# Kernel tuning notes

Measured on AMD Instinct MI355X. Metric: run time of the kernel, lower is better.

Reference implementation:

```python
import jax, jax.numpy as jnp
import numpy as np

ALPHA = 3.0   # config.model.hgnn_alpha
K = 16        # config.model.k_neighbors
S, N, E, D = 3, 8192, 1024, 512


def setup_inputs() -> dict:
    key = jax.random.key(0)
    k1, k2, k3 = jax.random.split(key, 3)
    x = jax.random.normal(k1, (1,), dtype=jnp.float32)  # only used for device in torch
    node_embed = jax.random.normal(k2, (S, N, D), dtype=jnp.float32)  # embednod tables
    edge_embed = jax.random.normal(k3, (S, E, D), dtype=jnp.float32)  # embedhy tables
    return {"x": x, "node_embed": node_embed, "edge_embed": edge_embed}


def reference(x, node_embed, edge_embed):
    # sim[s] = n_embed @ h_embed.T  -> [S, N, E]
    sim = jnp.einsum('snd,sed->sne', node_embed, edge_embed)
    # adj = softmax(relu(alpha * sim), dim=1 over hyperedges)
    adj = jax.nn.softmax(jax.nn.relu(ALPHA * sim), axis=-1)
    # top-k mask along hyperedge axis (scatter 1s at top-k indices per row)
    _, topk_idx = jax.lax.top_k(adj, K)  # [S, N, K]
    s_idx = jnp.arange(S)[:, None, None]
    n_idx = jnp.arange(N)[None, :, None]
    mask = jnp.zeros_like(adj).at[s_idx, n_idx, topk_idx].set(1.0)
    adj = adj * mask
    # hard threshold: binary incidence matrix per scale.
    # Original then drops all-zero hyperedge columns and returns nonzero
    # (node_idx, hyperedge_idx) pairs -- data-dependent shapes, so the dense
    # binary incidence [S, N, E] is the jit-compatible equivalent output;
    # the index lists are exactly its nonzero coordinates.
    hard = jnp.where(adj > 0.5, 1.0, 0.0)
    return hard
```

## Files before the change

kernel.cpp:

```cpp
#include <hip/hip_runtime.h>
#include <cmath>

#define SS 3
#define NN 8192
#define EE 1024
#define DD 512
#define ALPHA 3.0f
#define TAU 0.03f

typedef __attribute__((ext_vector_type(8))) short bf16x8;
typedef __attribute__((ext_vector_type(4))) float f32x4;

#define AS1(p) ((const __attribute__((address_space(1))) void*)(p))
#define AS3(p) ((__attribute__((address_space(3))) void*)(p))

__device__ __forceinline__ unsigned short f2bf(float x) {
    unsigned u = __float_as_uint(x);
    return (unsigned short)((u + 0x7fffu + ((u >> 16) & 1u)) >> 16);
}
__device__ __forceinline__ float bf2f(unsigned short h) {
    return __uint_as_float(((unsigned)h) << 16);
}

__device__ __forceinline__ void gload_lds16(const unsigned short* g, unsigned short* l) {
    __builtin_amdgcn_global_load_lds(AS1(g), AS3(l), 16, 0, 0);
}

__global__ __launch_bounds__(256)
void split_both_kernel(const float* __restrict__ node, const float* __restrict__ edge,
                       unsigned short* __restrict__ Ah, unsigned short* __restrict__ Al,
                       unsigned short* __restrict__ Bh, unsigned short* __restrict__ Bl)
{
    const int nA = SS * NN * DD / 4;
    const int nB = SS * EE * DD / 4;
    int i = blockIdx.x * blockDim.x + threadIdx.x;

    const float4* src;
    unsigned short* hi;
    unsigned short* lo;
    int idx;
    if (i < nA) {
        src = (const float4*)node; hi = Ah; lo = Al; idx = i;
    } else if (i < nA + nB) {
        src = (const float4*)edge; hi = Bh; lo = Bl; idx = i - nA;
    } else {
        return;
    }
    float4 v = src[idx];
    ushort4 h, l;
    h.x = f2bf(v.x); l.x = f2bf(v.x - bf2f(h.x));
    h.y = f2bf(v.y); l.y = f2bf(v.y - bf2f(h.y));
    h.z = f2bf(v.z); l.z = f2bf(v.z - bf2f(h.z));
    h.w = f2bf(v.w); l.w = f2bf(v.w - bf2f(h.w));
    ((ushort4*)hi)[idx] = h;
    ((ushort4*)lo)[idx] = l;
}

__global__ __launch_bounds__(256)
void gemm_mfma_kernel(const unsigned short* __restrict__ Ah,
                      const unsigned short* __restrict__ Al,
                      const unsigned short* __restrict__ Bh,
                      const unsigned short* __restrict__ Bl,
                      float* __restrict__ out)
{
    const int s  = blockIdx.z;
    const int m0 = blockIdx.x * 128;
    const int n0 = blockIdx.y * 128;

    const unsigned short* pAh = Ah + (size_t)s * NN * DD;
    const unsigned short* pAl = Al + (size_t)s * NN * DD;
    const unsigned short* pBh = Bh + (size_t)s * EE * DD;
    const unsigned short* pBl = Bl + (size_t)s * EE * DD;
    float* C = out + (size_t)s * NN * EE;

    __shared__ unsigned short lds[2 * 1024 * 8];

    const int t    = threadIdx.x;
    const int lane = t & 63;
    const int wid  = t >> 6;
    const int wm   = wid >> 1;
    const int wn   = wid & 1;
    const int fr   = lane & 15;
    const int kg   = lane >> 4;

    f32x4 acc[4][4];
#pragma unroll
    for (int i = 0; i < 4; ++i)
#pragma unroll
        for (int j = 0; j < 4; ++j) acc[i][j] = (f32x4){0.f, 0.f, 0.f, 0.f};

    for (int k0 = 0; k0 < DD; k0 += 32) {
#pragma unroll
        for (int i = 0; i < 8; ++i) {
            const int c    = i * 256 + t;
            const int pc   = c & 1023;
            const int row  = pc >> 3;
            const int slot = pc & 7;
            const int j    = slot ^ (row & 7);
            const unsigned short* src;
            if (c < 1024) {
                src = (j < 4) ? pAh + (size_t)(m0 + row) * DD + k0 + j * 8
                              : pAl + (size_t)(m0 + row) * DD + k0 + (j - 4) * 8;
            } else {
                src = (j < 4) ? pBh + (size_t)(n0 + row) * DD + k0 + j * 8
                              : pBl + (size_t)(n0 + row) * DD + k0 + (j - 4) * 8;
            }
            gload_lds16(src, &lds[c * 8]);
        }
        __syncthreads();

        bf16x8 ah[4], al[4], bh[4], bl[4];
#pragma unroll
        for (int i = 0; i < 4; ++i) {
            const int r = wm * 64 + i * 16 + fr;
            ah[i] = *(const bf16x8*)&lds[r * 64 + ((kg)     ^ (r & 7)) * 8];
            al[i] = *(const bf16x8*)&lds[r * 64 + ((4 + kg) ^ (r & 7)) * 8];
        }
#pragma unroll
        for (int j = 0; j < 4; ++j) {
            const int r = wn * 64 + j * 16 + fr;
            bh[j] = *(const bf16x8*)&lds[8192 + r * 64 + ((kg)     ^ (r & 7)) * 8];
            bl[j] = *(const bf16x8*)&lds[8192 + r * 64 + ((4 + kg) ^ (r & 7)) * 8];
        }
#pragma unroll
        for (int i = 0; i < 4; ++i)
#pragma unroll
            for (int j = 0; j < 4; ++j) {
                acc[i][j] = __builtin_amdgcn_mfma_f32_16x16x32_bf16(ah[i], bh[j], acc[i][j], 0, 0, 0);
                acc[i][j] = __builtin_amdgcn_mfma_f32_16x16x32_bf16(ah[i], bl[j], acc[i][j], 0, 0, 0);
                acc[i][j] = __builtin_amdgcn_mfma_f32_16x16x32_bf16(al[i], bh[j], acc[i][j], 0, 0, 0);
            }
        __syncthreads();
    }

#pragma unroll
    for (int i = 0; i < 4; ++i)
#pragma unroll
        for (int j = 0; j < 4; ++j) {
            const int col = n0 + wn * 64 + j * 16 + fr;
#pragma unroll
            for (int r = 0; r < 4; ++r) {
                const int row = m0 + wm * 64 + i * 16 + kg * 4 + r;
                C[(size_t)row * EE + col] = fmaxf(ALPHA * acc[i][j][r], 0.f);
            }
        }
}

__global__ void zero_count_kernel(int* __restrict__ count) {
    if (threadIdx.x == 0 && blockIdx.x == 0) count[0] = 0;
}

__global__ __launch_bounds__(256)
void softmax_threshold_flag_kernel(float* __restrict__ out,
                                   int* __restrict__ count,
                                   int* __restrict__ worklist)
{
    const int wave = threadIdx.x >> 6;
    const int lane = threadIdx.x & 63;
    const size_t row = (size_t)blockIdx.x * 4 + wave;
    float* p = out + row * EE;

    float z[16];
    float m = 0.f;
#pragma unroll
    for (int j = 0; j < 4; ++j) {
        float4 v = *(const float4*)(p + j * 256 + lane * 4);
        z[j*4+0] = v.x; z[j*4+1] = v.y; z[j*4+2] = v.z; z[j*4+3] = v.w;
        m = fmaxf(m, fmaxf(fmaxf(v.x, v.y), fmaxf(v.z, v.w)));
    }
#pragma unroll
    for (int off = 32; off >= 1; off >>= 1)
        m = fmaxf(m, __shfl_xor(m, off, 64));

    float e[16];
    float sum = 0.f;
#pragma unroll
    for (int j = 0; j < 16; ++j) {
        e[j] = expf(z[j] - m);
        sum += e[j];
    }
#pragma unroll
    for (int off = 32; off >= 1; off >>= 1)
        sum += __shfl_xor(sum, off, 64);

    const float thr = 0.5f * sum;
    const float T   = m + logf(thr);
    int lf = 0;
#pragma unroll
    for (int j = 0; j < 16; ++j)
        lf |= (fabsf(z[j] - T) < TAU) ? 1 : 0;

#pragma unroll
    for (int j = 0; j < 4; ++j) {
        float4 o;
        o.x = (e[j*4+0] > thr) ? 1.f : 0.f;
        o.y = (e[j*4+1] > thr) ? 1.f : 0.f;
        o.z = (e[j*4+2] > thr) ? 1.f : 0.f;
        o.w = (e[j*4+3] > thr) ? 1.f : 0.f;
        *(float4*)(p + j * 256 + lane * 4) = o;
    }
    const int anyf = __any(lf);
    if (anyf && lane == 0) {
        int idx = atomicAdd(count, 1);
        worklist[idx] = (int)row;
    }
}

__global__ __launch_bounds__(256)
void fixup_z_kernel(const float* __restrict__ node, const float* __restrict__ edge,
                    const int* __restrict__ count, const int* __restrict__ worklist,
                    float* __restrict__ zbuf, int zcap)
{
    __shared__ float sa[DD];
    const int t    = threadIdx.x;
    const int lane = t & 63;
    const int wid  = t >> 6;

    int nwork = count[0];
    if (nwork > zcap) nwork = zcap;
    const int items = nwork * 4;

    for (int item = blockIdx.x; item < items; item += gridDim.x) {
        const int w   = item >> 2;
        const int row = worklist[w];
        const int c0  = (item & 3) * 256;
        const int s   = row / NN;
        const float* a = node + (size_t)row * DD;
        const float* B = edge + (size_t)s * EE * DD;

        __syncthreads();
        if (t < DD / 4) ((float4*)sa)[t] = ((const float4*)a)[t];
        __syncthreads();

        const float4 va0 = ((const float4*)sa)[lane];
        const float4 va1 = ((const float4*)sa)[64 + lane];

        const int cbase = c0 + wid * 64;
        for (int g = 0; g < 16; ++g) {
            float acc[4];
#pragma unroll
            for (int j = 0; j < 4; ++j) {
                const float* b = B + (size_t)(cbase + g * 4 + j) * DD;
                float4 b0 = *(const float4*)(b + lane * 4);
                float4 b1 = *(const float4*)(b + 256 + lane * 4);
                float av;
                av = va0.x * b0.x;
                av = fmaf(va0.y, b0.y, av);
                av = fmaf(va0.z, b0.z, av);
                av = fmaf(va0.w, b0.w, av);
                av = fmaf(va1.x, b1.x, av);
                av = fmaf(va1.y, b1.y, av);
                av = fmaf(va1.z, b1.z, av);
                av = fmaf(va1.w, b1.w, av);
                acc[j] = av;
            }
#pragma unroll
            for (int off = 32; off >= 1; off >>= 1) {
#pragma unroll
                for (int j = 0; j < 4; ++j)
                    acc[j] += __shfl_xor(acc[j], off, 64);
            }
            if (lane == 0) {
#pragma unroll
                for (int j = 0; j < 4; ++j)
                    zbuf[(size_t)w * EE + cbase + g * 4 + j] = fmaxf(ALPHA * acc[j], 0.f);
            }
        }
    }
}

__global__ __launch_bounds__(256)
void fixup_finish_kernel(const float* __restrict__ zbuf,
                         const int* __restrict__ count, const int* __restrict__ worklist,
                         float* __restrict__ out, int zcap)
{
    const int lane = threadIdx.x & 63;
    const int wid  = threadIdx.x >> 6;
    int nwork = count[0];
    if (nwork > zcap) nwork = zcap;

    for (int w = blockIdx.x * 4 + wid; w < nwork; w += gridDim.x * 4) {
        const int row = worklist[w];
        const float* p = zbuf + (size_t)w * EE;

        float z[16];
        float m = 0.f;
#pragma unroll
        for (int j = 0; j < 4; ++j) {
            float4 v = *(const float4*)(p + j * 256 + lane * 4);
            z[j*4+0] = v.x; z[j*4+1] = v.y; z[j*4+2] = v.z; z[j*4+3] = v.w;
            m = fmaxf(m, fmaxf(fmaxf(v.x, v.y), fmaxf(v.z, v.w)));
        }
#pragma unroll
        for (int off = 32; off >= 1; off >>= 1)
            m = fmaxf(m, __shfl_xor(m, off, 64));

        float e[16], sum = 0.f;
#pragma unroll
        for (int j = 0; j < 16; ++j) { e[j] = expf(z[j] - m); sum += e[j]; }
#pragma unroll
        for (int off = 32; off >= 1; off >>= 1)
            sum += __shfl_xor(sum, off, 64);

        const float thr = 0.5f * sum;
        float* q = out + (size_t)row * EE;
#pragma unroll
        for (int j = 0; j < 4; ++j) {
            float4 o;
            o.x = (e[j*4+0] > thr) ? 1.f : 0.f;
            o.y = (e[j*4+1] > thr) ? 1.f : 0.f;
            o.z = (e[j*4+2] > thr) ? 1.f : 0.f;
            o.w = (e[j*4+3] > thr) ? 1.f : 0.f;
            *(float4*)(q + j * 256 + lane * 4) = o;
        }
    }
}

__global__ __launch_bounds__(256)
void fixup2_kernel(const float* __restrict__ node, const float* __restrict__ edge,
                   const int* __restrict__ count, const int* __restrict__ worklist,
                   float* __restrict__ out, int start)
{
    __shared__ float sa[DD];
    __shared__ float zrow[EE];
    __shared__ float red[8];

    const int t    = threadIdx.x;
    const int lane = t & 63;
    const int wid  = t >> 6;
    const int nwork = count[0];

    for (int w = start + blockIdx.x; w < nwork; w += gridDim.x) {
        const int row = worklist[w];
        const int s = row / NN;
        const float* a = node + (size_t)row * DD;
        const float* B = edge + (size_t)s * EE * DD;

        __syncthreads();
        if (t < DD / 4) ((float4*)sa)[t] = ((const float4*)a)[t];
        __syncthreads();

        float4 va0 = ((const float4*)sa)[lane];
        float4 va1 = ((const float4*)sa)[64 + lane];

        for (int c = wid; c < EE; c += 4) {
            const float* b = B + (size_t)c * DD;
            float4 b0 = *(const float4*)(b + lane * 4);
            float4 b1 = *(const float4*)(b + 256 + lane * 4);
            float acc;
            acc = va0.x * b0.x;
            acc = fmaf(va0.y, b0.y, acc);
            acc = fmaf(va0.z, b0.z, acc);
            acc = fmaf(va0.w, b0.w, acc);
            acc = fmaf(va1.x, b1.x, acc);
            acc = fmaf(va1.y, b1.y, acc);
            acc = fmaf(va1.z, b1.z, acc);
            acc = fmaf(va1.w, b1.w, acc);
#pragma unroll
            for (int off = 32; off >= 1; off >>= 1)
                acc += __shfl_xor(acc, off, 64);
            if (lane == 0) zrow[c] = fmaxf(ALPHA * acc, 0.f);
        }
        __syncthreads();

        float z[4], m = 0.f;
#pragma unroll
        for (int j = 0; j < 4; ++j) {
            z[j] = zrow[j * 256 + t];
            m = fmaxf(m, z[j]);
        }
#pragma unroll
        for (int off = 32; off >= 1; off >>= 1)
            m = fmaxf(m, __shfl_xor(m, off, 64));
        if (lane == 0) red[wid] = m;
        __syncthreads();
        m = fmaxf(fmaxf(red[0], red[1]), fmaxf(red[2], red[3]));

        float e[4], sum = 0.f;
#pragma unroll
        for (int j = 0; j < 4; ++j) { e[j] = expf(z[j] - m); sum += e[j]; }
#pragma unroll
        for (int off = 32; off >= 1; off >>= 1)
            sum += __shfl_xor(sum, off, 64);
        if (lane == 0) red[4 + wid] = sum;
        __syncthreads();
        sum = red[4] + red[5] + red[6] + red[7];

        const float thr = 0.5f * sum;
#pragma unroll
        for (int j = 0; j < 4; ++j)
            out[(size_t)row * EE + j * 256 + t] = (e[j] > thr) ? 1.f : 0.f;
        __syncthreads();
    }
}

#define BM 128
#define BN 128
#define BK 16
#define TM 8
#define TN 8

__global__ __launch_bounds__(256, 2)
void gemm_relu_kernel(const float* __restrict__ node,
                      const float* __restrict__ edge,
                      float* __restrict__ out)
{
    const int s  = blockIdx.z;
    const int m0 = blockIdx.y * BM;
    const int n0 = blockIdx.x * BN;

    const float* A = node + (size_t)s * NN * DD;
    const float* B = edge + (size_t)s * EE * DD;
    float*       C = out  + (size_t)s * NN * EE;

    __shared__ float As[BK][BM + 4];
    __shared__ float Bs[BK][BN + 4];

    const int tid = threadIdx.x;
    const int tx  = tid % 16;
    const int ty  = tid / 16;
    const int lrow = tid / 4;
    const int lcol = (tid % 4) * 4;

    float acc[TM][TN];
#pragma unroll
    for (int i = 0; i < TM; ++i)
#pragma unroll
        for (int j = 0; j < TN; ++j) acc[i][j] = 0.f;

    for (int k0 = 0; k0 < DD; k0 += BK) {
#pragma unroll
        for (int p = 0; p < 2; ++p) {
            const int r = lrow + p * 64;
            float4 v = *(const float4*)(A + (size_t)(m0 + r) * DD + k0 + lcol);
            As[lcol + 0][r] = v.x; As[lcol + 1][r] = v.y;
            As[lcol + 2][r] = v.z; As[lcol + 3][r] = v.w;
            float4 w = *(const float4*)(B + (size_t)(n0 + r) * DD + k0 + lcol);
            Bs[lcol + 0][r] = w.x; Bs[lcol + 1][r] = w.y;
            Bs[lcol + 2][r] = w.z; Bs[lcol + 3][r] = w.w;
        }
        __syncthreads();
#pragma unroll
        for (int k = 0; k < BK; ++k) {
            float a[TM], b[TN];
            float4 a0 = *(const float4*)&As[k][ty * 8];
            float4 a1 = *(const float4*)&As[k][ty * 8 + 4];
            a[0]=a0.x; a[1]=a0.y; a[2]=a0.z; a[3]=a0.w;
            a[4]=a1.x; a[5]=a1.y; a[6]=a1.z; a[7]=a1.w;
            float4 b0 = *(const float4*)&Bs[k][tx * 8];
            float4 b1 = *(const float4*)&Bs[k][tx * 8 + 4];
            b[0]=b0.x; b[1]=b0.y; b[2]=b0.z; b[3]=b0.w;
            b[4]=b1.x; b[5]=b1.y; b[6]=b1.z; b[7]=b1.w;
#pragma unroll
            for (int i = 0; i < TM; ++i)
#pragma unroll
                for (int j = 0; j < TN; ++j)
                    acc[i][j] = fmaf(a[i], b[j], acc[i][j]);
        }
        __syncthreads();
    }
#pragma unroll
    for (int i = 0; i < TM; ++i) {
        const size_t row = (size_t)(m0 + ty * 8 + i);
        float4 o0, o1;
        o0.x = fmaxf(ALPHA * acc[i][0], 0.f);
        o0.y = fmaxf(ALPHA * acc[i][1], 0.f);
        o0.z = fmaxf(ALPHA * acc[i][2], 0.f);
        o0.w = fmaxf(ALPHA * acc[i][3], 0.f);
        o1.x = fmaxf(ALPHA * acc[i][4], 0.f);
        o1.y = fmaxf(ALPHA * acc[i][5], 0.f);
        o1.z = fmaxf(ALPHA * acc[i][6], 0.f);
        o1.w = fmaxf(ALPHA * acc[i][7], 0.f);
        *(float4*)(C + row * EE + n0 + tx * 8)     = o0;
        *(float4*)(C + row * EE + n0 + tx * 8 + 4) = o1;
    }
}

__global__ __launch_bounds__(256)
void softmax_threshold_kernel(float* __restrict__ out)
{
    const int wave = threadIdx.x >> 6;
    const int lane = threadIdx.x & 63;
    const size_t row = (size_t)blockIdx.x * 4 + wave;
    float* p = out + row * EE;

    float z[16];
    float m = 0.f;
#pragma unroll
    for (int j = 0; j < 4; ++j) {
        float4 v = *(const float4*)(p + j * 256 + lane * 4);
        z[j*4+0] = v.x; z[j*4+1] = v.y; z[j*4+2] = v.z; z[j*4+3] = v.w;
        m = fmaxf(m, fmaxf(fmaxf(v.x, v.y), fmaxf(v.z, v.w)));
    }
#pragma unroll
    for (int off = 32; off >= 1; off >>= 1)
        m = fmaxf(m, __shfl_xor(m, off, 64));
    float e[16], sum = 0.f;
#pragma unroll
    for (int j = 0; j < 16; ++j) { e[j] = expf(z[j] - m); sum += e[j]; }
#pragma unroll
    for (int off = 32; off >= 1; off >>= 1)
        sum += __shfl_xor(sum, off, 64);
    const float thr = 0.5f * sum;
#pragma unroll
    for (int j = 0; j < 4; ++j) {
        float4 o;
        o.x = (e[j*4+0] > thr) ? 1.f : 0.f;
        o.y = (e[j*4+1] > thr) ? 1.f : 0.f;
        o.z = (e[j*4+2] > thr) ? 1.f : 0.f;
        o.w = (e[j*4+3] > thr) ? 1.f : 0.f;
        *(float4*)(p + j * 256 + lane * 4) = o;
    }
}

extern "C" void kernel_launch(void* const* d_in, const int* in_sizes, int n_in,
                              void* d_out, int out_size, void* d_ws, size_t ws_size,
                              hipStream_t stream) {
    const float* node = (const float*)d_in[1];
    const float* edge = (const float*)d_in[2];
    float* out = (float*)d_out;

    const size_t SAe = (size_t)SS * NN * DD;
    const size_t SBe = (size_t)SS * EE * DD;
    const size_t split_bytes = (2 * SAe + 2 * SBe) * 2;
    const size_t wl_bytes    = (size_t)(SS * NN + 1) * 4;
    const size_t base_need   = split_bytes + wl_bytes;

    if (ws_size >= base_need) {
        unsigned short* Ah = (unsigned short*)d_ws;
        unsigned short* Al = Ah + SAe;
        unsigned short* Bh = Al + SAe;
        unsigned short* Bl = Bh + SBe;
        int* count    = (int*)(Bl + SBe);
        int* worklist = count + 1;

        const size_t zoff = (base_need + 255) & ~(size_t)255;
        int zcap = 0;
        if (ws_size > zoff) {
            size_t zc = (ws_size - zoff) / ((size_t)EE * 4);
            zcap = (int)(zc > 4096 ? 4096 : zc);
        }
        float* zbuf = (float*)((char*)d_ws + zoff);

        const int n4 = (int)((SAe + SBe) / 4);
        split_both_kernel<<<(n4 + 255) / 256, 256, 0, stream>>>(node, edge, Ah, Al, Bh, Bl);

        zero_count_kernel<<<1, 64, 0, stream>>>(count);

        dim3 g1(NN / 128, EE / 128, SS);
        gemm_mfma_kernel<<<g1, 256, 0, stream>>>(Ah, Al, Bh, Bl, out);

        softmax_threshold_flag_kernel<<<(SS * NN) / 4, 256, 0, stream>>>(out, count, worklist);

        if (zcap > 0) {
            fixup_z_kernel<<<1024, 256, 0, stream>>>(node, edge, count, worklist, zbuf, zcap);
            fixup_finish_kernel<<<64, 256, 0, stream>>>(zbuf, count, worklist, out, zcap);
        }
        fixup2_kernel<<<512, 256, 0, stream>>>(node, edge, count, worklist, out, zcap);
    } else {
        dim3 g1(EE / BN, NN / BM, SS);
        gemm_relu_kernel<<<g1, 256, 0, stream>>>(node, edge, out);
        softmax_threshold_kernel<<<(SS * NN) / 4, 256, 0, stream>>>(out);
    }
}
```

Before: 151.2 us.

## Enlarge GEMM tile to 256x256 with 8 waves and double-buffered LDS

After: 153.9 us. No clear change (+1.8%).

```diff
diff --git a/kernel.cpp b/kernel.cpp
--- a/kernel.cpp
+++ b/kernel.cpp
@@ -56,7 +56,7 @@
     ((ushort4*)lo)[idx] = l;
 }
 
-__global__ __launch_bounds__(256)
+__global__ __launch_bounds__(512, 2)
 void gemm_mfma_kernel(const unsigned short* __restrict__ Ah,
                       const unsigned short* __restrict__ Al,
                       const unsigned short* __restrict__ Bh,
@@ -64,8 +64,8 @@
                       float* __restrict__ out)
 {
     const int s  = blockIdx.z;
-    const int m0 = blockIdx.x * 128;
-    const int n0 = blockIdx.y * 128;
+    const int m0 = blockIdx.x * 256;
+    const int n0 = blockIdx.y * 256;
 
     const unsigned short* pAh = Ah + (size_t)s * NN * DD;
     const unsigned short* pAl = Al + (size_t)s * NN * DD;
@@ -73,74 +73,86 @@
     const unsigned short* pBl = Bl + (size_t)s * EE * DD;
     float* C = out + (size_t)s * NN * EE;
 
-    __shared__ unsigned short lds[2 * 1024 * 8];
+    __shared__ unsigned short lds[2 * 512 * 64];
 
     const int t    = threadIdx.x;
     const int lane = t & 63;
     const int wid  = t >> 6;
-    const int wm   = wid >> 1;
-    const int wn   = wid & 1;
+    const int wm   = wid >> 2;
+    const int wn   = wid & 3;
     const int fr   = lane & 15;
     const int kg   = lane >> 4;
 
-    f32x4 acc[4][4];
-#pragma unroll
-    for (int i = 0; i < 4; ++i)
+    f32x4 acc[8][4];
+#pragma unroll
+    for (int i = 0; i < 8; ++i)
 #pragma unroll
         for (int j = 0; j < 4; ++j) acc[i][j] = (f32x4){0.f, 0.f, 0.f, 0.f};
 
-    for (int k0 = 0; k0 < DD; k0 += 32) {
+    auto stage = [&](int buf, int k0) {
 #pragma unroll
         for (int i = 0; i < 8; ++i) {
-            const int c    = i * 256 + t;
-            const int pc   = c & 1023;
-            const int row  = pc >> 3;
-            const int slot = pc & 7;
+            const int c    = i * 512 + t;
+            const int row  = c >> 3;
+            const int slot = c & 7;
             const int j    = slot ^ (row & 7);
             const unsigned short* src;
-            if (c < 1024) {
+            if (row < 256) {
                 src = (j < 4) ? pAh + (size_t)(m0 + row) * DD + k0 + j * 8
                               : pAl + (size_t)(m0 + row) * DD + k0 + (j - 4) * 8;
             } else {
-                src = (j < 4) ? pBh + (size_t)(n0 + row) * DD + k0 + j * 8
-                              : pBl + (size_t)(n0 + row) * DD + k0 + (j - 4) * 8;
+                const int rn = row - 256;
+                src = (j < 4) ? pBh + (size_t)(n0 + rn) * DD + k0 + j * 8
+                              : pBl + (size_t)(n0 + rn) * DD + k0 + (j - 4) * 8;
             }
-            gload_lds16(src, &lds[c * 8]);
-        }
-        __syncthreads();
-
-        bf16x8 ah[4], al[4], bh[4], bl[4];
-#pragma unroll
-        for (int i = 0; i < 4; ++i) {
-            const int r = wm * 64 + i * 16 + fr;
-            ah[i] = *(const bf16x8*)&lds[r * 64 + ((kg)     ^ (r & 7)) * 8];
-            al[i] = *(const bf16x8*)&lds[r * 64 + ((4 + kg) ^ (r & 7)) * 8];
-        }
+            gload_lds16(src, &lds[buf * 32768 + c * 8]);
+        }
+    };
+
+    auto compute = [&](int buf) {
+        const unsigned short* L = &lds[buf * 32768];
+        bf16x8 bh[4], bl[4];
 #pragma unroll
         for (int j = 0; j < 4; ++j) {
-            const int r = wn * 64 + j * 16 + fr;
-            bh[j] = *(const bf16x8*)&lds[8192 + r * 64 + ((kg)     ^ (r & 7)) * 8];
-            bl[j] = *(const bf16x8*)&lds[8192 + r * 64 + ((4 + kg) ^ (r & 7)) * 8];
-        }
-#pragma unroll
-        for (int i = 0; i < 4; ++i)
+            const int r = 256 + wn * 64 + j * 16 + fr;
+            bh[j] = *(const bf16x8*)&L[r * 64 + ((kg)     ^ (r & 7)) * 8];
+            bl[j] = *(const bf16x8*)&L[r * 64 + ((4 + kg) ^ (r & 7)) * 8];
+        }
+        __builtin_amdgcn_s_setprio(1);
+#pragma unroll
+        for (int i = 0; i < 8; ++i) {
+            const int r = wm * 128 + i * 16 + fr;
+            bf16x8 ah = *(const bf16x8*)&L[r * 64 + ((kg)     ^ (r & 7)) * 8];
+            bf16x8 al = *(const bf16x8*)&L[r * 64 + ((4 + kg) ^ (r & 7)) * 8];
 #pragma unroll
             for (int j = 0; j < 4; ++j) {
-                acc[i][j] = __builtin_amdgcn_mfma_f32_16x16x32_bf16(ah[i], bh[j], acc[i][j], 0, 0, 0);
-                acc[i][j] = __builtin_amdgcn_mfma_f32_16x16x32_bf16(ah[i], bl[j], acc[i][j], 0, 0, 0);
-                acc[i][j] = __builtin_amdgcn_mfma_f32_16x16x32_bf16(al[i], bh[j], acc[i][j], 0, 0, 0);
+                acc[i][j] = __builtin_amdgcn_mfma_f32_16x16x32_bf16(ah, bh[j], acc[i][j], 0, 0, 0);
+                acc[i][j] = __builtin_amdgcn_mfma_f32_16x16x32_bf16(ah, bl[j], acc[i][j], 0, 0, 0);
+                acc[i][j] = __builtin_amdgcn_mfma_f32_16x16x32_bf16(al, bh[j], acc[i][j], 0, 0, 0);
             }
-        __syncthreads();
-    }
-
-#pragma unroll
-    for (int i = 0; i < 4; ++i)
+        }
+        __builtin_amdgcn_s_setprio(0);
+    };
+
+    stage(0, 0);
+    __syncthreads();
+
+#pragma unroll 1
+    for (int ks = 0; ks < 15; ++ks) {
+        stage((ks + 1) & 1, (ks + 1) * 32);
+        compute(ks & 1);
+        __syncthreads();
+    }
+    compute(15 & 1);
+
+#pragma unroll
+    for (int i = 0; i < 8; ++i)
 #pragma unroll
         for (int j = 0; j < 4; ++j) {
             const int col = n0 + wn * 64 + j * 16 + fr;
 #pragma unroll
             for (int r = 0; r < 4; ++r) {
-                const int row = m0 + wm * 64 + i * 16 + kg * 4 + r;
+                const int row = m0 + wm * 128 + i * 16 + kg * 4 + r;
                 C[(size_t)row * EE + col] = fmaxf(ALPHA * acc[i][j][r], 0.f);
             }
         }
@@ -547,8 +559,8 @@
 
         zero_count_kernel<<<1, 64, 0, stream>>>(count);
 
-        dim3 g1(NN / 128, EE / 128, SS);
-        gemm_mfma_kernel<<<g1, 256, 0, stream>>>(Ah, Al, Bh, Bl, out);
+        dim3 g1(NN / 256, EE / 256, SS);
+        gemm_mfma_kernel<<<g1, 512, 0, stream>>>(Ah, Al, Bh, Bl, out);
 
         softmax_threshold_flag_kernel<<<(SS * NN) / 4, 256, 0, stream>>>(out, count, worklist);
 
```

## Switch split-bf16 GEMM to 32x32x16 MFMA with fragment-ordered LDS layout

Applied to the files above, without the earlier changes.

After: 183.1 us. 21.1% more time.

```diff
diff --git a/kernel.cpp b/kernel.cpp
--- a/kernel.cpp
+++ b/kernel.cpp
@@ -10,6 +10,7 @@
 
 typedef __attribute__((ext_vector_type(8))) short bf16x8;
 typedef __attribute__((ext_vector_type(4))) float f32x4;
+typedef __attribute__((ext_vector_type(16))) float f32x16;
 
 #define AS1(p) ((const __attribute__((address_space(1))) void*)(p))
 #define AS3(p) ((__attribute__((address_space(3))) void*)(p))
@@ -73,75 +74,80 @@
     const unsigned short* pBl = Bl + (size_t)s * EE * DD;
     float* C = out + (size_t)s * NN * EE;
 
-    __shared__ unsigned short lds[2 * 1024 * 8];
+    __shared__ unsigned short lds[32 * 512];
 
     const int t    = threadIdx.x;
     const int lane = t & 63;
     const int wid  = t >> 6;
     const int wm   = wid >> 1;
     const int wn   = wid & 1;
-    const int fr   = lane & 15;
-    const int kg   = lane >> 4;
-
-    f32x4 acc[4][4];
-#pragma unroll
-    for (int i = 0; i < 4; ++i)
-#pragma unroll
-        for (int j = 0; j < 4; ++j) acc[i][j] = (f32x4){0.f, 0.f, 0.f, 0.f};
+    const int fr   = lane & 31;
+    const int kp   = lane >> 5;
+
+    f32x16 acc[2][2];
+#pragma unroll
+    for (int p = 0; p < 2; ++p)
+#pragma unroll
+        for (int nf = 0; nf < 2; ++nf)
+#pragma unroll
+            for (int r = 0; r < 16; ++r) acc[p][nf][r] = 0.f;
 
     for (int k0 = 0; k0 < DD; k0 += 32) {
 #pragma unroll
         for (int i = 0; i < 8; ++i) {
-            const int c    = i * 256 + t;
-            const int pc   = c & 1023;
-            const int row  = pc >> 3;
-            const int slot = pc & 7;
-            const int j    = slot ^ (row & 7);
+            const int c = wid * 8 + i;
             const unsigned short* src;
-            if (c < 1024) {
-                src = (j < 4) ? pAh + (size_t)(m0 + row) * DD + k0 + j * 8
-                              : pAl + (size_t)(m0 + row) * DD + k0 + (j - 4) * 8;
+            if (c < 16) {
+                const int pl = c >> 3;
+                const int ks = (c >> 2) & 1;
+                const int mf = c & 3;
+                src = (pl ? pAl : pAh) + (size_t)(m0 + mf * 32 + fr) * DD + k0 + ks * 16 + kp * 8;
             } else {
-                src = (j < 4) ? pBh + (size_t)(n0 + row) * DD + k0 + j * 8
-                              : pBl + (size_t)(n0 + row) * DD + k0 + (j - 4) * 8;
+                const int c2 = c - 16;
+                const int pl = c2 >> 3;
+                const int ks = (c2 >> 2) & 1;
+                const int nf = c2 & 3;
+                src = (pl ? pBl : pBh) + (size_t)(n0 + nf * 32 + fr) * DD + k0 + ks * 16 + kp * 8;
             }
-            gload_lds16(src, &lds[c * 8]);
-        }
-        __syncthreads();
-
-        bf16x8 ah[4], al[4], bh[4], bl[4];
-#pragma unroll
-        for (int i = 0; i < 4; ++i) {
-            const int r = wm * 64 + i * 16 + fr;
-            ah[i] = *(const bf16x8*)&lds[r * 64 + ((kg)     ^ (r & 7)) * 8];
-            al[i] = *(const bf16x8*)&lds[r * 64 + ((4 + kg) ^ (r & 7)) * 8];
-        }
-#pragma unroll
-        for (int j = 0; j < 4; ++j) {
-            const int r = wn * 64 + j * 16 + fr;
-            bh[j] = *(const bf16x8*)&lds[8192 + r * 64 + ((kg)     ^ (r & 7)) * 8];
-            bl[j] = *(const bf16x8*)&lds[8192 + r * 64 + ((4 + kg) ^ (r & 7)) * 8];
-        }
-#pragma unroll
-        for (int i = 0; i < 4; ++i)
-#pragma unroll
-            for (int j = 0; j < 4; ++j) {
-                acc[i][j] = __builtin_amdgcn_mfma_f32_16x16x32_bf16(ah[i], bh[j], acc[i][j], 0, 0, 0);
-                acc[i][j] = __builtin_amdgcn_mfma_f32_16x16x32_bf16(ah[i], bl[j], acc[i][j], 0, 0, 0);
-                acc[i][j] = __builtin_amdgcn_mfma_f32_16x16x32_bf16(al[i], bh[j], acc[i][j], 0, 0, 0);
-            }
-        __syncthreads();
-    }
-
-#pragma unroll
-    for (int i = 0; i < 4; ++i)
-#pragma unroll
-        for (int j = 0; j < 4; ++j) {
-            const int col = n0 + wn * 64 + j * 16 + fr;
-#pragma unroll
-            for (int r = 0; r < 4; ++r) {
-                const int row = m0 + wm * 64 + i * 16 + kg * 4 + r;
-                C[(size_t)row * EE + col] = fmaxf(ALPHA * acc[i][j][r], 0.f);
+            gload_lds16(src, &lds[c * 512 + lane * 8]);
+        }
+        __syncthreads();
+
+#pragma unroll
+        for (int ks = 0; ks < 2; ++ks) {
+            bf16x8 a[2][2], b[2][2];
+#pragma unroll
+            for (int p = 0; p < 2; ++p)
+#pragma unroll
+                for (int pl = 0; pl < 2; ++pl)
+                    a[p][pl] = *(const bf16x8*)&lds[(pl * 8 + ks * 4 + (wm * 2 + p)) * 512 + lane * 8];
+#pragma unroll
+            for (int nf = 0; nf < 2; ++nf)
+#pragma unroll
+                for (int pl = 0; pl < 2; ++pl)
+                    b[nf][pl] = *(const bf16x8*)&lds[(16 + pl * 8 + ks * 4 + (wn * 2 + nf)) * 512 + lane * 8];
+
+#pragma unroll
+            for (int p = 0; p < 2; ++p)
+#pragma unroll
+                for (int nf = 0; nf < 2; ++nf) {
+                    acc[p][nf] = __builtin_amdgcn_mfma_f32_32x32x16_bf16(a[p][0], b[nf][0], acc[p][nf], 0, 0, 0);
+                    acc[p][nf] = __builtin_amdgcn_mfma_f32_32x32x16_bf16(a[p][0], b[nf][1], acc[p][nf], 0, 0, 0);
+                    acc[p][nf] = __builtin_amdgcn_mfma_f32_32x32x16_bf16(a[p][1], b[nf][0], acc[p][nf], 0, 0, 0);
+                }
+        }
+        __syncthreads();
+    }
+
+#pragma unroll
+    for (int p = 0; p < 2; ++p)
+#pragma unroll
+        for (int nf = 0; nf < 2; ++nf) {
+            const int col = n0 + wn * 64 + nf * 32 + fr;
+#pragma unroll
+            for (int r = 0; r < 16; ++r) {
+                const int row = m0 + wm * 64 + p * 32 + (r & 3) + 8 * (r >> 2) + 4 * kp;
+                C[(size_t)row * EE + col] = fmaxf(ALPHA * acc[p][nf][r], 0.f);
             }
         }
 }
```
